# Kernel tuning notes

Measured on AMD Instinct MI355X. Metric: run time of the kernel, lower is better.

The kernel has to match this reference:

```python
import jax, jax.numpy as jnp
import numpy as np

B, S, D, E, K = 4, 2048, 1024, 8, 2
H = 4 * D  # SwiGLU hidden size


def setup_inputs() -> dict:
    key = jax.random.key(0)
    ks = jax.random.split(key, 6)
    s = 0.02
    return {
        "x": jax.random.normal(ks[0], (B, S, D), dtype=jnp.float32),
        "Wr": jax.random.normal(ks[1], (D, E), dtype=jnp.float32) * s,
        "br": jnp.zeros((E,), jnp.float32),
        "Wg": jax.random.normal(ks[2], (E, D, H), dtype=jnp.float32) * s,
        "bg": jnp.zeros((E, H), jnp.float32),
        "Wu": jax.random.normal(ks[3], (E, D, H), dtype=jnp.float32) * s,
        "bu": jnp.zeros((E, H), jnp.float32),
        "Wd": jax.random.normal(ks[4], (E, H, D), dtype=jnp.float32) * s,
        "bd": jnp.zeros((E, D), jnp.float32),
        "top_k": K,
    }


def reference(x, Wr, br, Wg, bg, Wu, bu, Wd, bd, top_k):
    # Router: top-k over expert logits, softmax over the selected k values.
    Bx, Sx, Dx = x.shape
    Ex = Wr.shape[-1]
    logits = x @ Wr + br                              # [B,S,E]
    vals, idx = jax.lax.top_k(logits, top_k)          # [B,S,K]
    probs = jax.nn.softmax(vals, axis=-1)             # [B,S,K]
    # Dense per-token expert weight; 0 for experts the token is not routed to.
    gate_w = jnp.sum(jax.nn.one_hot(idx, Ex, dtype=x.dtype) * probs[..., None], axis=-2)  # [B,S,E]

    xt = x.reshape(-1, Dx)          # [T,D]
    gw = gate_w.reshape(-1, Ex).T   # [E,T]

    def body(acc, p):
        wg, bgi, wu, bui, wd, bdi, ge = p
        h = jax.nn.silu(xt @ wg + bgi) * (xt @ wu + bui)   # [T,4D]
        y = (h @ wd + bdi) * ge[:, None]                   # zero where ge==0 (not routed)
        return acc + y, None

    out, _ = jax.lax.scan(body, jnp.zeros_like(xt), (Wg, bg, Wu, bu, Wd, bd, gw))
    return out.reshape(Bx, Sx, Dx)
```

## Files before the change

### kernel.cpp

```cpp
#include <hip/hip_runtime.h>
#include <hip/hip_fp16.h>


#define T_TOK 8192
#define D_IN  1024
#define E_EXP 8
#define H_HID 4096
#define NSLOT (T_TOK * 2)
#define NSLOT_PAD (NSLOT + 256)

typedef _Float16 f16;
typedef __attribute__((ext_vector_type(8))) _Float16 f16x8;
typedef __attribute__((ext_vector_type(4))) _Float16 f16x4;
typedef __attribute__((ext_vector_type(4))) float f32x4;

__device__ __forceinline__ void gload_lds16(const void* g, void* l) {
  __builtin_amdgcn_global_load_lds(
      (const __attribute__((address_space(1))) unsigned int*)g,
      (__attribute__((address_space(3))) unsigned int*)l, 16, 0, 0);
}

template<int MAP>
__global__ __launch_bounds__(256) void transpose_cvt_kernel(
    const float* __restrict__ src, f16* __restrict__ dst, int R, int C,
    size_t dstride) {
  __shared__ float tile[32][33];
  int b = blockIdx.z;
  const float* s = src + (size_t)b * R * C;
  f16* d = dst + (size_t)b * dstride;
  int c0 = blockIdx.x * 32, r0 = blockIdx.y * 32;
  int tr = threadIdx.x >> 3;
  int tc4 = (threadIdx.x & 7) * 4;
  float4 v = *(const float4*)(s + (size_t)(r0 + tr) * C + c0 + tc4);
  tile[tr][tc4 + 0] = v.x;
  tile[tr][tc4 + 1] = v.y;
  tile[tr][tc4 + 2] = v.z;
  tile[tr][tc4 + 3] = v.w;
  __syncthreads();
  int c = c0 + tr;
  int ro = (MAP == 0) ? c : (((c >> 4) << 5) + ((MAP == 2) ? 16 : 0) + (c & 15));
  f16x4 o = {(f16)tile[tc4 + 0][tr], (f16)tile[tc4 + 1][tr],
             (f16)tile[tc4 + 2][tr], (f16)tile[tc4 + 3][tr]};
  *(f16x4*)(d + (size_t)ro * R + r0 + tc4) = o;
}


__global__ __launch_bounds__(256) void router_kernel(
    const float* __restrict__ x, const float* __restrict__ Wr,
    const float* __restrict__ br, int* __restrict__ eidx,
    float2* __restrict__ pval, int* __restrict__ counts,
    f16* __restrict__ xb) {
  int lane = threadIdx.x & 63, wid = threadIdx.x >> 6;
  int t = blockIdx.x * 4 + wid;
  const float* xr = x + (size_t)t * D_IN;
  float s[8] = {0.f, 0.f, 0.f, 0.f, 0.f, 0.f, 0.f, 0.f};
  int dbase = lane * 16;
#pragma unroll
  for (int i = 0; i < 4; ++i) {
    float4 xv = *(const float4*)(xr + dbase + i * 4);
    f16x4 xo = {(f16)xv.x, (f16)xv.y, (f16)xv.z, (f16)xv.w};
    *(f16x4*)(xb + (size_t)t * D_IN + dbase + i * 4) = xo;
    const float xs[4] = {xv.x, xv.y, xv.z, xv.w};
#pragma unroll
    for (int j = 0; j < 4; ++j) {
      const float* wr = Wr + (size_t)(dbase + i * 4 + j) * E_EXP;
      float4 w0 = *(const float4*)wr;
      float4 w1 = *(const float4*)(wr + 4);
      float xvj = xs[j];
      s[0] += xvj * w0.x; s[1] += xvj * w0.y; s[2] += xvj * w0.z; s[3] += xvj * w0.w;
      s[4] += xvj * w1.x; s[5] += xvj * w1.y; s[6] += xvj * w1.z; s[7] += xvj * w1.w;
    }
  }
#pragma unroll
  for (int off = 32; off; off >>= 1)
#pragma unroll
    for (int e = 0; e < 8; ++e) s[e] += __shfl_xor(s[e], off);
  if (lane == 0) {
    float v[8];
#pragma unroll
    for (int e = 0; e < 8; ++e) v[e] = s[e] + br[e];
    int i0 = 0; float v0 = v[0];
#pragma unroll
    for (int e = 1; e < 8; ++e) if (v[e] > v0) { v0 = v[e]; i0 = e; }
    int i1 = -1; float v1 = -1e30f;
#pragma unroll
    for (int e = 0; e < 8; ++e)
      if (e != i0 && v[e] > v1) { v1 = v[e]; i1 = e; }
    float ed = __expf(v1 - v0);
    float inv = 1.f / (1.f + ed);
    eidx[t] = i0 | (i1 << 8);
    pval[t] = make_float2(inv, ed * inv);
    atomicAdd(&counts[i0], 1);
    atomicAdd(&counts[i1], 1);
  }
}

__global__ void scan_kernel(const int* __restrict__ counts, int* __restrict__ offsets) {
  if (threadIdx.x == 0) {
    int acc = 0;
#pragma unroll
    for (int e = 0; e < E_EXP; ++e) { offsets[e] = acc; acc += counts[e]; }
    offsets[E_EXP] = acc;
  }
}

__global__ __launch_bounds__(256) void scatter_kernel(
    const int* __restrict__ eidx, const float2* __restrict__ pval,
    const int* __restrict__ offsets, int* __restrict__ cursors,
    int* __restrict__ perm, float* __restrict__ gatew, int2* __restrict__ slotAB) {
  int t = blockIdx.x * 256 + threadIdx.x;
  if (t >= T_TOK) return;
  int ei = eidx[t];
  float2 p = pval[t];
  int e0 = ei & 0xff, e1 = (ei >> 8) & 0xff;
  int s0 = offsets[e0] + atomicAdd(&cursors[e0], 1);
  perm[s0] = t; gatew[s0] = p.x;
  int s1 = offsets[e1] + atomicAdd(&cursors[e1], 1);
  perm[s1] = t; gatew[s1] = p.y;
  slotAB[t] = make_int2(s0, s1);
}


#define SB0 __builtin_amdgcn_sched_barrier(0)
#define BAR do { SB0; __builtin_amdgcn_s_barrier(); SB0; } while (0)
#define VMCNT(N) asm volatile("s_waitcnt vmcnt(" #N ")" ::: "memory")

#define STAGE_(B, ISB, H, KT, BASE) do {                                   \
  char* d_ = smem + (B)*65536 + (ISB)*32768 + (H)*16384 + wid*1024;        \
  gload_lds16(BASE[(H)*2+0] + (size_t)(KT)*64, d_);                        \
  gload_lds16(BASE[(H)*2+1] + (size_t)(KT)*64, d_ + 8192);                 \
} while (0)

#define LDA_(B, Q)                                                          \
  _Pragma("unroll")                                                         \
  for (int m_ = 0; m_ < 4; ++m_) {                                          \
    fa[m_][0] = *(const f16x8*)(smem + (B)*65536 + aoff + ((Q)*4+m_)*2048 + offk0); \
    fa[m_][1] = *(const f16x8*)(smem + (B)*65536 + aoff + ((Q)*4+m_)*2048 + offk1); \
  }

#define LDB_(FB, B, RH)                                                     \
  _Pragma("unroll")                                                         \
  for (int n_ = 0; n_ < 2; ++n_) {                                          \
    FB[n_][0] = *(const f16x8*)(smem + (B)*65536 + 32768 + boff + ((RH)*2+n_)*2048 + offk0); \
    FB[n_][1] = *(const f16x8*)(smem + (B)*65536 + 32768 + boff + ((RH)*2+n_)*2048 + offk1); \
  }

#define QUAD_(Q, RH, FB)                                                    \
  __builtin_amdgcn_s_setprio(1);                                            \
  _Pragma("unroll")                                                         \
  for (int m_ = 0; m_ < 4; ++m_)                                            \
    _Pragma("unroll")                                                       \
    for (int n_ = 0; n_ < 2; ++n_) {                                        \
      acc[(Q)*4+m_][(RH)*2+n_] = __builtin_amdgcn_mfma_f32_16x16x32_f16(    \
          fa[m_][0], FB[n_][0], acc[(Q)*4+m_][(RH)*2+n_], 0, 0, 0);         \
      acc[(Q)*4+m_][(RH)*2+n_] = __builtin_amdgcn_mfma_f32_16x16x32_f16(    \
          fa[m_][1], FB[n_][1], acc[(Q)*4+m_][(RH)*2+n_], 0, 0, 0);         \
    }                                                                       \
  __builtin_amdgcn_s_setprio(0);

template<int MODE>
__global__ __launch_bounds__(512, 2) void ffn_8ph_kernel(
    const f16* __restrict__ Asrc, const f16* __restrict__ Bsrc,
    const float* __restrict__ bias0, const float* __restrict__ bias1,
    const int* __restrict__ offsets, const int* __restrict__ perm,
    const float* __restrict__ gatew, f16* __restrict__ dst) {
  constexpr int KD = MODE ? H_HID : D_IN;
  constexpr int BROWS = MODE ? D_IN : 2 * H_HID;
  constexpr int NT = KD / 64;
  static_assert(NT % 2 == 0, "NT even");

  __shared__ __align__(16) char smem[131072];

  int g = blockIdx.x;
  int xcd = g & 7;
  int mt = (g >> 3) & 31;
  int panel = xcd + 8 * (g >> 8);
  int e, nt;
  if constexpr (MODE == 0) { e = panel >> 5; nt = panel & 31; }
  else                     { e = panel >> 2; nt = panel & 3; }

  int off = offsets[e];
  int cnt = offsets[e + 1] - off;
  if (mt * 256 >= cnt) return;

  int tid = threadIdx.x, lane = tid & 63, wid = tid >> 6;
  int wm = wid >> 2, wn = wid & 3;
  int l15 = lane & 15, lc0 = lane >> 4, s7 = l15 & 7;
  int aoff = (wm * 128 + l15) * 128;
  int boff = (wn * 64 + l15) * 128;
  int offk0 = ((lc0) ^ s7) * 16;
  int offk1 = ((lc0 + 4) ^ s7) * 16;

  int rowh_[2], lc_[2];
#pragma unroll
  for (int i = 0; i < 2; ++i) {
    int chunk = (i * 8 + wid) * 64 + lane;
    rowh_[i] = chunk >> 3;
    lc_[i] = (chunk & 7) ^ (rowh_[i] & 7);
  }

  const f16 *aB[4], *bB[4];
#pragma unroll
  for (int h = 0; h < 2; ++h)
#pragma unroll
    for (int i = 0; i < 2; ++i) {
      int absrow = h * 128 + rowh_[i];
      bB[h * 2 + i] =
          Bsrc + ((size_t)e * BROWS + nt * 256 + absrow) * KD + lc_[i] * 8;
      int slot = off + min(mt * 256 + absrow, cnt - 1);
      if constexpr (MODE == 0)
        aB[h * 2 + i] = Asrc + (size_t)perm[slot] * KD + lc_[i] * 8;
      else
        aB[h * 2 + i] = Asrc + (size_t)slot * KD + lc_[i] * 8;
    }

  float bv0[4], bv1[2];
  if constexpr (MODE == 0) {
#pragma unroll
    for (int p = 0; p < 2; ++p) {
      int h = nt * 128 + wn * 32 + p * 16 + l15;
      bv0[p] = bias0[e * H_HID + h];
      bv1[p] = bias1[e * H_HID + h];
    }
  } else {
#pragma unroll
    for (int n = 0; n < 4; ++n)
      bv0[n] = bias0[e * D_IN + nt * 256 + wn * 64 + n * 16 + l15];
  }

  f32x4 acc[8][4] = {};
  f16x8 fa[4][2], fb01[2][2], fb23[2][2];

  STAGE_(0, 1, 0, 0, bB); STAGE_(0, 1, 1, 0, bB);
  STAGE_(0, 0, 0, 0, aB); STAGE_(0, 0, 1, 0, aB);
  STAGE_(1, 1, 0, 1, bB); STAGE_(1, 1, 1, 1, bB);
  STAGE_(1, 0, 0, 1, aB);
  VMCNT(6);
  BAR;

  for (int it = 0; it < NT / 2; ++it) {
    int b_ = 2 * it + 1;
    int a2 = min(2 * it + 2, NT - 1);
    int b2 = min(2 * it + 3, NT - 1);
    LDA_(0, 0); LDB_(fb01, 0, 0); STAGE_(1, 0, 1, b_, aB);
    BAR; QUAD_(0, 0, fb01); BAR;
    LDB_(fb23, 0, 1);
    BAR; QUAD_(0, 1, fb23); BAR;
    LDA_(0, 1); STAGE_(0, 1, 0, a2, bB);
    BAR; QUAD_(1, 0, fb01); BAR;
    STAGE_(0, 1, 1, a2, bB);
    BAR; QUAD_(1, 1, fb23);
    VMCNT(4);
    BAR;
    LDA_(1, 0); LDB_(fb01, 1, 0); STAGE_(0, 0, 0, a2, aB);
    BAR; QUAD_(0, 0, fb01); BAR;
    LDB_(fb23, 1, 1); STAGE_(0, 0, 1, a2, aB);
    BAR; QUAD_(0, 1, fb23); BAR;
    LDA_(1, 1); STAGE_(1, 1, 0, b2, bB);
    BAR; QUAD_(1, 0, fb01); BAR;
    STAGE_(1, 1, 1, b2, bB); STAGE_(1, 0, 0, b2, aB);
    BAR; QUAD_(1, 1, fb23);
    VMCNT(6);
    BAR;
  }

  int c0_ = lc0 * 4;
  if constexpr (MODE == 0) {
#pragma unroll
    for (int p = 0; p < 2; ++p) {
      int h = nt * 128 + wn * 32 + p * 16 + l15;
#pragma unroll
      for (int m = 0; m < 8; ++m) {
        int lbase = mt * 256 + wm * 128 + m * 16 + c0_;
#pragma unroll
        for (int r = 0; r < 4; ++r) {
          if (lbase + r < cnt) {
            float gv = acc[m][2 * p][r] + bv0[p];
            float uv = acc[m][2 * p + 1][r] + bv1[p];
            __builtin_nontemporal_store(
                (f16)((gv / (1.f + __expf(-gv))) * uv),
                &dst[(size_t)(off + lbase + r) * H_HID + h]);
          }
        }
      }
    }
  } else {
#pragma unroll
    for (int n = 0; n < 4; ++n) {
      int col = nt * 256 + wn * 64 + n * 16 + l15;
#pragma unroll
      for (int m = 0; m < 8; ++m) {
        int lbase = mt * 256 + wm * 128 + m * 16 + c0_;
#pragma unroll
        for (int r = 0; r < 4; ++r) {
          if (lbase + r < cnt) {
            int slot = off + lbase + r;
            __builtin_nontemporal_store(
                (f16)(gatew[slot] * (acc[m][n][r] + bv0[n])),
                &dst[(size_t)slot * D_IN + col]);
          }
        }
      }
    }
  }
}

__global__ __launch_bounds__(256) void combine_kernel(
    const f16* __restrict__ ybuf, const int2* __restrict__ slotAB,
    float* __restrict__ out) {
  int i = blockIdx.x * 256 + threadIdx.x;
  int t = i >> 7;
  int c8 = i & 127;
  int2 s = slotAB[t];
  f16x8 y0 = *(const f16x8*)(ybuf + (size_t)s.x * D_IN + c8 * 8);
  f16x8 y1 = *(const f16x8*)(ybuf + (size_t)s.y * D_IN + c8 * 8);
  float* o = out + (size_t)t * D_IN + c8 * 8;
  f32x4 o0 = {(float)y0[0] + (float)y1[0], (float)y0[1] + (float)y1[1],
              (float)y0[2] + (float)y1[2], (float)y0[3] + (float)y1[3]};
  f32x4 o1 = {(float)y0[4] + (float)y1[4], (float)y0[5] + (float)y1[5],
              (float)y0[6] + (float)y1[6], (float)y0[7] + (float)y1[7]};
  __builtin_nontemporal_store(o0, (f32x4*)o);
  __builtin_nontemporal_store(o1, (f32x4*)(o + 4));
}


extern "C" void kernel_launch(void* const* d_in, const int* in_sizes, int n_in,
                              void* d_out, int out_size, void* d_ws, size_t ws_size,
                              hipStream_t stream) {
  const float* x  = (const float*)d_in[0];
  const float* Wr = (const float*)d_in[1];
  const float* br = (const float*)d_in[2];
  const float* Wg = (const float*)d_in[3];
  const float* bg = (const float*)d_in[4];
  const float* Wu = (const float*)d_in[5];
  const float* bu = (const float*)d_in[6];
  const float* Wd = (const float*)d_in[7];
  const float* bd = (const float*)d_in[8];
  float* out = (float*)d_out;

  char* ws = (char*)d_ws;
  size_t o = 0;
  auto alloc = [&](size_t bytes) {
    size_t r = o;
    o += (bytes + 255) & ~(size_t)255;
    return r;
  };
  f16* xb     = (f16*)(ws + alloc((size_t)T_TOK * D_IN * 2));
  f16* wgut   = (f16*)(ws + alloc((size_t)E_EXP * 2 * H_HID * D_IN * 2));
  f16* wdt    = (f16*)(ws + alloc((size_t)E_EXP * D_IN * H_HID * 2));
  f16* hbuf   = (f16*)(ws + alloc((size_t)NSLOT_PAD * H_HID * 2));
  int* eidx   = (int*)(ws + alloc((size_t)T_TOK * 4));
  float2* pval= (float2*)(ws + alloc((size_t)T_TOK * 8));
  int* counts = (int*)(ws + alloc(64 * 4));
  int* cursors = counts + 8;
  int* offsets = counts + 16;
  int* perm   = (int*)(ws + alloc((size_t)NSLOT_PAD * 4));
  float* gatew= (float*)(ws + alloc((size_t)NSLOT_PAD * 4));
  int2* slotAB= (int2*)(ws + alloc((size_t)T_TOK * 8));
  f16* ybuf   = wgut;

  hipMemsetAsync(counts, 0, 64 * 4, stream);

  router_kernel<<<T_TOK / 4, 256, 0, stream>>>(x, Wr, br, eidx, pval, counts, xb);
  scan_kernel<<<1, 64, 0, stream>>>(counts, offsets);
  scatter_kernel<<<T_TOK / 256, 256, 0, stream>>>(eidx, pval, offsets, cursors,
                                                  perm, gatew, slotAB);
  transpose_cvt_kernel<1><<<dim3(H_HID / 32, D_IN / 32, E_EXP), 256, 0, stream>>>(
      Wg, wgut, D_IN, H_HID, (size_t)2 * H_HID * D_IN);
  transpose_cvt_kernel<2><<<dim3(H_HID / 32, D_IN / 32, E_EXP), 256, 0, stream>>>(
      Wu, wgut, D_IN, H_HID, (size_t)2 * H_HID * D_IN);
  ffn_8ph_kernel<0><<<dim3(8192), 512, 0, stream>>>(
      xb, wgut, bg, bu, offsets, perm, nullptr, hbuf);
  transpose_cvt_kernel<0><<<dim3(D_IN / 32, H_HID / 32, E_EXP), 256, 0, stream>>>(
      Wd, wdt, H_HID, D_IN, (size_t)D_IN * H_HID);
  ffn_8ph_kernel<1><<<dim3(1024), 512, 0, stream>>>(
      hbuf, wdt, bd, nullptr, offsets, nullptr, gatew, ybuf);
  combine_kernel<<<T_TOK * D_IN / 8 / 256, 256, 0, stream>>>(ybuf, slotAB, out);
}
```

Measured before the change: 1.003 ms.

## Split down-projection GEMM along K with fp32 atomic accumulation

The down-projection kernel now splits the 4096-long hidden dimension into four 1024-wide chunks, launching four times as many blocks so that more CUs have work when experts hold only a few token tiles. Each chunk adds its gated partial result into a zeroed fp32 slot buffer with atomicAdd, and only chunk 0 adds the bias. The combine kernel then reads fp32 partials instead of fp16. The cost is an extra large memset, atomic write traffic about four times the old output size, and doubled read traffic in the combine step.

Measured after the change: 1.169 ms. 16.5% more time.

```diff
diff --git a/kernel.cpp b/kernel.cpp
--- a/kernel.cpp
+++ b/kernel.cpp
@@ -163,21 +163,25 @@
     const f16* __restrict__ Asrc, const f16* __restrict__ Bsrc,
     const float* __restrict__ bias0, const float* __restrict__ bias1,
     const int* __restrict__ offsets, const int* __restrict__ perm,
-    const float* __restrict__ gatew, f16* __restrict__ dst) {
+    const float* __restrict__ gatew, f16* __restrict__ dst,
+    float* __restrict__ dst32) {
   constexpr int KD = MODE ? H_HID : D_IN;
   constexpr int BROWS = MODE ? D_IN : 2 * H_HID;
-  constexpr int NT = KD / 64;
-  static_assert(NT % 2 == 0, "NT even");
+  constexpr int NT = 16;
 
   __shared__ __align__(16) char smem[131072];
 
   int g = blockIdx.x;
   int xcd = g & 7;
   int mt = (g >> 3) & 31;
-  int panel = xcd + 8 * (g >> 8);
-  int e, nt;
-  if constexpr (MODE == 0) { e = panel >> 5; nt = panel & 31; }
-  else                     { e = panel >> 2; nt = panel & 3; }
+  int e, nt, kc;
+  if constexpr (MODE == 0) {
+    int panel = xcd + 8 * (g >> 8);
+    e = panel >> 5; nt = panel & 31; kc = 0;
+  } else {
+    int sp = xcd + 8 * (g >> 8);
+    e = sp >> 4; nt = (sp >> 2) & 3; kc = sp & 3;
+  }
 
   int off = offsets[e];
   int cnt = offsets[e + 1] - off;
@@ -205,13 +209,13 @@
 #pragma unroll
     for (int i = 0; i < 2; ++i) {
       int absrow = h * 128 + rowh_[i];
-      bB[h * 2 + i] =
-          Bsrc + ((size_t)e * BROWS + nt * 256 + absrow) * KD + lc_[i] * 8;
+      bB[h * 2 + i] = Bsrc + ((size_t)e * BROWS + nt * 256 + absrow) * KD +
+                      kc * 1024 + lc_[i] * 8;
       int slot = off + min(mt * 256 + absrow, cnt - 1);
       if constexpr (MODE == 0)
         aB[h * 2 + i] = Asrc + (size_t)perm[slot] * KD + lc_[i] * 8;
       else
-        aB[h * 2 + i] = Asrc + (size_t)slot * KD + lc_[i] * 8;
+        aB[h * 2 + i] = Asrc + (size_t)slot * KD + kc * 1024 + lc_[i] * 8;
     }
 
   float bv0[4], bv1[2];
@@ -225,7 +229,9 @@
   } else {
 #pragma unroll
     for (int n = 0; n < 4; ++n)
-      bv0[n] = bias0[e * D_IN + nt * 256 + wn * 64 + n * 16 + l15];
+      bv0[n] = (kc == 0)
+                   ? bias0[e * D_IN + nt * 256 + wn * 64 + n * 16 + l15]
+                   : 0.f;
   }
 
   f32x4 acc[8][4] = {};
@@ -295,9 +301,8 @@
         for (int r = 0; r < 4; ++r) {
           if (lbase + r < cnt) {
             int slot = off + lbase + r;
-            __builtin_nontemporal_store(
-                (f16)(gatew[slot] * (acc[m][n][r] + bv0[n])),
-                &dst[(size_t)slot * D_IN + col]);
+            atomicAdd(&dst32[(size_t)slot * D_IN + col],
+                      gatew[slot] * (acc[m][n][r] + bv0[n]));
           }
         }
       }
@@ -306,19 +311,18 @@
 }
 
 __global__ __launch_bounds__(256) void combine_kernel(
-    const f16* __restrict__ ybuf, const int2* __restrict__ slotAB,
+    const float* __restrict__ ybuf32, const int2* __restrict__ slotAB,
     float* __restrict__ out) {
   int i = blockIdx.x * 256 + threadIdx.x;
   int t = i >> 7;
   int c8 = i & 127;
   int2 s = slotAB[t];
-  f16x8 y0 = *(const f16x8*)(ybuf + (size_t)s.x * D_IN + c8 * 8);
-  f16x8 y1 = *(const f16x8*)(ybuf + (size_t)s.y * D_IN + c8 * 8);
+  f32x4 a0 = *(const f32x4*)(ybuf32 + (size_t)s.x * D_IN + c8 * 8);
+  f32x4 a1 = *(const f32x4*)(ybuf32 + (size_t)s.x * D_IN + c8 * 8 + 4);
+  f32x4 b0 = *(const f32x4*)(ybuf32 + (size_t)s.y * D_IN + c8 * 8);
+  f32x4 b1 = *(const f32x4*)(ybuf32 + (size_t)s.y * D_IN + c8 * 8 + 4);
   float* o = out + (size_t)t * D_IN + c8 * 8;
-  f32x4 o0 = {(float)y0[0] + (float)y1[0], (float)y0[1] + (float)y1[1],
-              (float)y0[2] + (float)y1[2], (float)y0[3] + (float)y1[3]};
-  f32x4 o1 = {(float)y0[4] + (float)y1[4], (float)y0[5] + (float)y1[5],
-              (float)y0[6] + (float)y1[6], (float)y0[7] + (float)y1[7]};
+  f32x4 o0 = a0 + b0, o1 = a1 + b1;
   __builtin_nontemporal_store(o0, (f32x4*)o);
   __builtin_nontemporal_store(o1, (f32x4*)(o + 4));
 }
@@ -357,7 +361,7 @@
   int* perm   = (int*)(ws + alloc((size_t)NSLOT_PAD * 4));
   float* gatew= (float*)(ws + alloc((size_t)NSLOT_PAD * 4));
   int2* slotAB= (int2*)(ws + alloc((size_t)T_TOK * 8));
-  f16* ybuf   = wgut;
+  float* ybuf32 = (float*)wgut;
 
   hipMemsetAsync(counts, 0, 64 * 4, stream);
 
@@ -370,10 +374,11 @@
   transpose_cvt_kernel<2><<<dim3(H_HID / 32, D_IN / 32, E_EXP), 256, 0, stream>>>(
       Wu, wgut, D_IN, H_HID, (size_t)2 * H_HID * D_IN);
   ffn_8ph_kernel<0><<<dim3(8192), 512, 0, stream>>>(
-      xb, wgut, bg, bu, offsets, perm, nullptr, hbuf);
+      xb, wgut, bg, bu, offsets, perm, nullptr, hbuf, nullptr);
   transpose_cvt_kernel<0><<<dim3(D_IN / 32, H_HID / 32, E_EXP), 256, 0, stream>>>(
       Wd, wdt, H_HID, D_IN, (size_t)D_IN * H_HID);
-  ffn_8ph_kernel<1><<<dim3(1024), 512, 0, stream>>>(
-      hbuf, wdt, bd, nullptr, offsets, nullptr, gatew, ybuf);
-  combine_kernel<<<T_TOK * D_IN / 8 / 256, 256, 0, stream>>>(ybuf, slotAB, out);
-}
+  hipMemsetAsync(ybuf32, 0, (size_t)NSLOT_PAD * D_IN * 4, stream);
+  ffn_8ph_kernel<1><<<dim3(4096), 512, 0, stream>>>(
+      hbuf, wdt, bd, nullptr, offsets, nullptr, gatew, nullptr, ybuf32);
+  combine_kernel<<<T_TOK * D_IN / 8 / 256, 256, 0, stream>>>(ybuf32, slotAB, out);
+}
```
